# Kernel tuning notes

Hardware: AMD Instinct MI355X
Metric: run time of the kernel (lower is better)

Reference implementation:

```python
import jax, jax.numpy as jnp
import numpy as np

STRIDES = (4, 8, 16, 32)   # featmap_strides (FPN levels)
TAU = 2.0                  # level-weight temperature (translate_to_linear_weight)
G = 4                      # n_groups
SP = 32                    # spatial_points
TP = 8                     # temporal_points == T frames
D = 256                    # query_dim == feat_channels
CG = D // G                # channels per group
EFF = CG                   # eff_in_dim == eff_out_dim in AdaptiveMixing
OUT_S = SP * 4             # out_points (spatial), out_multiplier = 4
OUT_T = TP * 4
B, Q, T, IMG = 4, 100, 8, 256


def _ln2(x, eps=1e-5):
    # F.layer_norm over the last TWO dims, no affine params
    mu = jnp.mean(x, axis=(-2, -1), keepdims=True)
    var = jnp.var(x, axis=(-2, -1), keepdims=True)
    return (x - mu) * jax.lax.rsqrt(var + eps)


def _ln(x, g, b, eps=1e-5):
    mu = jnp.mean(x, axis=-1, keepdims=True)
    var = jnp.var(x, axis=-1, keepdims=True)
    return (x - mu) * jax.lax.rsqrt(var + eps) * g + b


def _bilinear(feat, px, py):
    # feat: [B,H,W,T,G,Cg]; px,py: [B,Q,G,S] pixel coords
    # grid_sample semantics: bilinear, align_corners=False, zero padding
    Bn, H, W, Tn, Gn, Cg = feat.shape
    bidx = jnp.arange(Bn)[:, None, None, None]
    gidx = jnp.arange(Gn)[None, None, :, None]
    x0 = jnp.floor(px); y0 = jnp.floor(py)
    fx = px - x0; fy = py - y0
    x0i = x0.astype(jnp.int32); y0i = y0.astype(jnp.int32)
    out = 0.0
    for dx, dy, w in ((0, 0, (1 - fx) * (1 - fy)), (1, 0, fx * (1 - fy)),
                      (0, 1, (1 - fx) * fy), (1, 1, fx * fy)):
        xi = x0i + dx; yi = y0i + dy
        valid = (xi >= 0) & (xi < W) & (yi >= 0) & (yi < H)
        xc = jnp.clip(xi, 0, W - 1); yc = jnp.clip(yi, 0, H - 1)
        v = feat[bidx, yc, xc, :, gidx, :]   # [B,Q,G,S,T,Cg]
        out = out + v * (w * valid)[..., None, None]
    return out


def _adaptive_mixing(x, query, Wp, bp, Wo, bo, n_in, n_out):
    # x: [B,Q,G,P,Cg]; per-instance dynamic channel mixing then point mixing
    Bn, Qn = x.shape[:2]
    params = (query @ Wp + bp).reshape(Bn, Qn, G, -1)
    M = params[..., :EFF * EFF].reshape(Bn, Qn, G, EFF, EFF)
    S = params[..., EFF * EFF:].reshape(Bn, Qn, G, n_out, n_in)
    out = jnp.einsum('bqgpc,bqgcd->bqgpd', x, M)
    out = jax.nn.relu(_ln2(out))
    out = jnp.einsum('bqgop,bqgpd->bqgod', S, out)
    out = jax.nn.relu(_ln2(out))
    out = out.reshape(Bn, Qn, -1) @ Wo + bo
    return query + out


def _forward(feat0, feat1, feat2, feat3, proposal_boxes, spatial_queries, temporal_queries,
             W_off, b_off, W_ps, b_ps, Wo_s, bo_s, g_s, be_s,
             W_pt, b_pt, Wo_t, bo_t, g_t, be_t):
    feats = (feat0, feat1, feat2, feat3)
    Bn, Qn, _ = spatial_queries.shape
    # offset_generator + make_sample_points (xyzr proposal boxes)
    off = (spatial_queries @ W_off + b_off).reshape(Bn, Qn, G * SP, 3)
    cc = proposal_boxes[..., None, :2]
    scale = 2.0 ** proposal_boxes[..., None, 2:3]
    r = proposal_boxes[..., None, 3:4]
    wh = scale * jnp.concatenate([2.0 ** (-0.5 * r), 2.0 ** (0.5 * r)], axis=-1)
    xy = (cc + off[..., :2] * wh).reshape(Bn, Qn, G, SP, 2)
    z = (proposal_boxes[..., None, 2] + off[..., 2]).reshape(Bn, Qn, G, SP)
    # soft level weights over log2-scale distance (translate_to_linear_weight)
    mapped = z - jnp.float32(float(np.log2(STRIDES[0])))
    lvls = jnp.arange(len(STRIDES), dtype=z.dtype)
    lw = jax.nn.softmax(-((mapped[..., None] - lvls) ** 2) / TAU, axis=-1)
    sampled = 0.0
    for i, feat in enumerate(feats):
        Bc, C, Tn, H, W = feat.shape
        fr = feat.transpose(0, 3, 4, 2, 1).reshape(Bc, H, W, Tn, G, CG)
        px = xy[..., 0] / STRIDES[i] - 0.5
        py = xy[..., 1] / STRIDES[i] - 0.5
        sampled = sampled + _bilinear(fr, px, py) * lw[..., i][..., None, None]
    sampled = sampled.transpose(0, 1, 2, 4, 3, 5)     # [B,Q,G,T,SP,Cg]
    spatial_feats = jnp.mean(sampled, axis=3)         # mean over T   -> [B,Q,G,SP,Cg]
    temporal_feats = jnp.mean(sampled, axis=4)        # mean over SP  -> [B,Q,G,T,Cg]
    sq = _adaptive_mixing(spatial_feats, spatial_queries, W_ps, b_ps, Wo_s, bo_s, SP, OUT_S)
    sq = _ln(sq, g_s, be_s)
    tq = _adaptive_mixing(temporal_feats, temporal_queries, W_pt, b_pt, Wo_t, bo_t, TP, OUT_T)
    tq = _ln(tq, g_t, be_t)
    return sq, tq


def setup_inputs() -> dict:
    key = jax.random.key(0)
    ks = jax.random.split(key, 24)
    f32 = jnp.float32
    inp = {}
    for i, s in enumerate(STRIDES):
        h = IMG // s
        inp['feat%d' % i] = jax.random.normal(ks[i], (B, D, T, h, h), dtype=f32)
    # xyzr boxes: center xy in image coords, z = log2 box scale, r = log2 aspect
    inp['proposal_boxes'] = jnp.concatenate([
        jax.random.uniform(ks[4], (B, Q, 2), dtype=f32) * IMG,
        jax.random.uniform(ks[5], (B, Q, 1), dtype=f32) * 3.0 + 3.0,
        jax.random.normal(ks[6], (B, Q, 1), dtype=f32) * 0.25,
    ], axis=-1)
    PS = EFF * EFF + SP * OUT_S
    PT = EFF * EFF + TP * OUT_T
    inp.update(
        spatial_queries=jax.random.normal(ks[7], (B, Q, D), dtype=f32),
        temporal_queries=jax.random.normal(ks[8], (B, Q, D), dtype=f32),
        W_off=jax.random.normal(ks[9], (D, SP * G * 3), dtype=f32) * 0.01,
        b_off=jax.random.normal(ks[10], (SP * G * 3,), dtype=f32) * 0.1,
        W_ps=jax.random.normal(ks[11], (D, G * PS), dtype=f32) * 0.02,
        b_ps=jax.random.normal(ks[12], (G * PS,), dtype=f32) * 0.02,
        Wo_s=jax.random.normal(ks[13], (G * EFF * OUT_S, D), dtype=f32) * 0.02,
        bo_s=jax.random.normal(ks[14], (D,), dtype=f32) * 0.02,
        g_s=jnp.ones((D,), dtype=f32),
        be_s=jnp.zeros((D,), dtype=f32),
        W_pt=jax.random.normal(ks[15], (D, G * PT), dtype=f32) * 0.02,
        b_pt=jax.random.normal(ks[16], (G * PT,), dtype=f32) * 0.02,
        Wo_t=jax.random.normal(ks[17], (G * EFF * OUT_T, D), dtype=f32) * 0.02,
        bo_t=jax.random.normal(ks[18], (D,), dtype=f32) * 0.02,
        g_t=jnp.ones((D,), dtype=f32),
        be_t=jnp.zeros((D,), dtype=f32),
    )
    return inp


def reference(feat0, feat1, feat2, feat3, proposal_boxes, spatial_queries, temporal_queries,
              W_off, b_off, W_ps, b_ps, Wo_s, bo_s, g_s, be_s,
              W_pt, b_pt, Wo_t, bo_t, g_t, be_t):
    return _forward(feat0, feat1, feat2, feat3, proposal_boxes, spatial_queries, temporal_queries,
                    W_off, b_off, W_ps, b_ps, Wo_s, bo_s, g_s, be_s,
                    W_pt, b_pt, Wo_t, bo_t, g_t, be_t)
```

## Files before the change

### kernel.cpp

```cpp
#include <hip/hip_runtime.h>
#include <hip/hip_bf16.h>


typedef __attribute__((ext_vector_type(8))) short bf16x8;
typedef __attribute__((ext_vector_type(8))) unsigned short u16x8;
typedef __attribute__((ext_vector_type(4))) float f32x4;

static __device__ __forceinline__ unsigned short f2bf(float f){
  unsigned u = __float_as_uint(f);
  u += 0x7fffu + ((u >> 16) & 1u);
  return (unsigned short)(u >> 16);
}
static __device__ __forceinline__ float bf2f(unsigned short h){
  return __uint_as_float(((unsigned)h) << 16);
}

__global__ __launch_bounds__(256) void k_wtrans_all(
    const float* __restrict__ Wps, const float* __restrict__ Wpt,
    const float* __restrict__ Wos, const float* __restrict__ Wot,
    unsigned short* __restrict__ WpsP, unsigned short* __restrict__ WptP,
    unsigned short* __restrict__ WosP, unsigned short* __restrict__ WotP,
    const float4* __restrict__ qs, const float4* __restrict__ qt,
    unsigned short* __restrict__ qsP, unsigned short* __restrict__ qtP){
  int id = blockIdx.x;
  if(id >= 5696){
    int blk = id - 5696;
    const float4* in; unsigned short* out; int i;
    if(blk < 100){ in = qs; out = qsP; i = blk*256 + threadIdx.x; }
    else         { in = qt; out = qtP; i = (blk-100)*256 + threadIdx.x; }
    float4 v = in[i];
    int row = i >> 6, k0 = (i & 63) * 4;
    int strip = row >> 4, colr = row & 15;
    int kk = k0 >> 5, kg = (k0 >> 3) & 3, e0 = k0 & 7;
    size_t dst = ((size_t)(strip*8 + kk)*64 + kg*16 + colr)*8 + e0;
    *(ushort4*)(out + dst) = make_ushort4(f2bf(v.x), f2bf(v.y), f2bf(v.z), f2bf(v.w));
    return;
  }
  const float* in; unsigned short* out; int N, KKtot, r0, c0;
  if(id < 2048){       in=Wps; out=WpsP; N=32768; KKtot=8;    c0=(id>>2)*64;        r0=(id&3)*64; }
  else if(id < 3136){ int i=id-2048; in=Wpt; out=WptP; N=17408; KKtot=8;    c0=(i>>2)*64; r0=(i&3)*64; }
  else if(id < 5184){ int i=id-3136; in=Wos; out=WosP; N=256;   KKtot=1024; c0=(i&3)*64;  r0=(i>>2)*64; }
  else {              int i=id-5184; in=Wot; out=WotP; N=256;   KKtot=256;  c0=(i&3)*64;  r0=(i>>2)*64; }
  __shared__ float tile[64][65];
  int lane = threadIdx.x & 63, wid = threadIdx.x >> 6;
  #pragma unroll
  for(int i=0;i<16;i++){
    int r = wid + 4*i;
    tile[r][lane] = in[(size_t)(r0 + r) * N + c0 + lane];
  }
  __syncthreads();
  int t = threadIdx.x;
  int ch = t >> 5, w2 = t & 31;
  int kk_l = ch >> 2, st_l = ch & 3;
  size_t chunkbase = ((size_t)((c0>>4) + st_l) * KKtot + ((r0>>5) + kk_l)) * 512;
  #pragma unroll
  for(int j=0;j<2;j++){
    int pl = w2*2 + j;
    int kg = pl >> 4, cc = pl & 15;
    u16x8 v;
    #pragma unroll
    for(int e=0;e<8;e++) v[e] = f2bf(tile[kk_l*32 + kg*8 + e][st_l*16 + cc]);
    *(u16x8*)(out + chunkbase + pl*8) = v;
  }
}

__global__ __launch_bounds__(384) void k_offsets(
    const float* __restrict__ q, const float* __restrict__ Woff,
    const float* __restrict__ boff, const float* __restrict__ boxes,
    float* __restrict__ xybuf, float* __restrict__ lwbuf){
  int bq = blockIdx.x;
  __shared__ float qsh[256];
  __shared__ float off[384];
  int tid = threadIdx.x;
  if(tid < 256) qsh[tid] = q[bq*256 + tid];
  __syncthreads();
  float acc = boff[tid];
  for(int k=0;k<256;k++) acc = fmaf(qsh[k], Woff[k*384 + tid], acc);
  off[tid] = acc;
  __syncthreads();
  if(tid < 128){
    float cx = boxes[bq*4+0], cy = boxes[bq*4+1];
    float zb = boxes[bq*4+2], r  = boxes[bq*4+3];
    float wx = exp2f(zb - 0.5f*r);
    float wy = exp2f(zb + 0.5f*r);
    float x = cx + off[tid*3+0]*wx;
    float y = cy + off[tid*3+1]*wy;
    float z = zb + off[tid*3+2];
    xybuf[(bq*128+tid)*2+0] = x;
    xybuf[(bq*128+tid)*2+1] = y;
    float m = z - 2.0f;
    float e0 = -0.5f*(m-0.f)*(m-0.f);
    float e1 = -0.5f*(m-1.f)*(m-1.f);
    float e2 = -0.5f*(m-2.f)*(m-2.f);
    float e3 = -0.5f*(m-3.f)*(m-3.f);
    float mx = fmaxf(fmaxf(e0,e1), fmaxf(e2,e3));
    float s0 = expf(e0-mx), s1 = expf(e1-mx), s2 = expf(e2-mx), s3 = expf(e3-mx);
    float inv = 1.0f/(s0+s1+s2+s3);
    lwbuf[(bq*128+tid)*4+0] = s0*inv;
    lwbuf[(bq*128+tid)*4+1] = s1*inv;
    lwbuf[(bq*128+tid)*4+2] = s2*inv;
    lwbuf[(bq*128+tid)*4+3] = s3*inv;
  }
}

__global__ __launch_bounds__(256) void k_feat_transpose_all(
    const float* __restrict__ f0, const float* __restrict__ f1,
    const float* __restrict__ f2, const float* __restrict__ f3,
    unsigned short* __restrict__ o0, unsigned short* __restrict__ o1,
    unsigned short* __restrict__ o2, unsigned short* __restrict__ o3){
  int px = blockIdx.x;
  const float* in; unsigned short* out; int P, p0;
  if(px < 64){      in=f0; out=o0; P=4096; p0=px*64; }
  else if(px < 80){ in=f1; out=o1; P=1024; p0=(px-64)*64; }
  else if(px < 84){ in=f2; out=o2; P=256;  p0=(px-80)*64; }
  else {            in=f3; out=o3; P=64;   p0=0; }
  __shared__ float tile[64][65];
  int c0 = blockIdx.y * 64;
  int b = blockIdx.z >> 3, t = blockIdx.z & 7;
  int tid = threadIdx.x;
  size_t inbase = ((size_t)b * 2048 + t) * (size_t)P;
  #pragma unroll
  for(int j=0;j<4;j++){
    int idx = j*256 + tid;
    int c = idx >> 4, q4 = idx & 15;
    float4 v = *(const float4*)(in + inbase + (size_t)(c0 + c) * 8 * P + p0 + q4*4);
    tile[c][q4*4+0] = v.x; tile[c][q4*4+1] = v.y;
    tile[c][q4*4+2] = v.z; tile[c][q4*4+3] = v.w;
  }
  __syncthreads();
  size_t outbase = (size_t)b * P * 2048 + (size_t)t * 256;
  #pragma unroll
  for(int j=0;j<4;j++){
    int idx = j*256 + tid;
    int p = idx >> 4, q4 = idx & 15;
    ushort4 o;
    o.x = f2bf(tile[q4*4+0][p]); o.y = f2bf(tile[q4*4+1][p]);
    o.z = f2bf(tile[q4*4+2][p]); o.w = f2bf(tile[q4*4+3][p]);
    *(ushort4*)(out + outbase + (size_t)(p0 + p) * 2048 + c0 + q4*4) = o;
  }
}

__global__ __launch_bounds__(256, 4) void k_sample_params(
    const unsigned short* __restrict__ f0, const unsigned short* __restrict__ f1,
    const unsigned short* __restrict__ f2, const unsigned short* __restrict__ f3,
    const float* __restrict__ xybuf, const float* __restrict__ lwbuf,
    float* __restrict__ sfeat, float* __restrict__ tfeat,
    const unsigned short* __restrict__ As, const unsigned short* __restrict__ WTs,
    const float* __restrict__ biass, unsigned short* __restrict__ outs,
    const unsigned short* __restrict__ At, const unsigned short* __restrict__ WTt,
    const float* __restrict__ biast, unsigned short* __restrict__ outt){
  if(blockIdx.x >= 1600){
    int flat = blockIdx.x - 1600;
    int nb = flat % 784, my = flat / 784;
    const unsigned short *A, *W; const float* bias; unsigned short* out; int N, nbl;
    if(nb < 512){ A=As; W=WTs; bias=biass; out=outs; N=32768; nbl=nb; }
    else        { A=At; W=WTt; bias=biast; out=outt; N=17408; nbl=nb-512; }
    int wave = threadIdx.x >> 6, lane = threadIdx.x & 63;
    int strip = nbl*4 + wave;
    int col = lane & 15, kg = lane >> 4;
    const bf16x8* wp = (const bf16x8*)W + (size_t)strip*8*64 + lane;
    bf16x8 bfrag[8];
    #pragma unroll
    for(int k=0;k<8;k++) bfrag[k] = wp[k*64];
    float bv = bias[strip*16 + col];
    int mt0 = my * 5;
    #pragma unroll
    for(int m=0; m<5; m++){
      int mt = mt0 + m;
      f32x4 acc = {bv, bv, bv, bv};
      const bf16x8* ap = (const bf16x8*)A + (size_t)mt*8*64 + lane;
      bf16x8 af[8];
      #pragma unroll
      for(int k=0;k<8;k++) af[k] = ap[k*64];
      #pragma unroll
      for(int k=0;k<8;k++)
        acc = __builtin_amdgcn_mfma_f32_16x16x32_bf16(af[k], bfrag[k], acc, 0, 0, 0);
      int rowb = mt*16 + kg*4;
      #pragma unroll
      for(int r=0;r<4;r++)
        out[(size_t)(rowb + r) * N + strip*16 + col] = f2bf(acc[r]);
    }
    return;
  }
  int bid = blockIdx.x;
  int g = bid & 3, bq = bid >> 2;
  int b = bq / 100;
  __shared__ unsigned smp[32][8][32];
  __shared__ int   soff[128][4];
  __shared__ float swt [128][4];
  int tid = threadIdx.x;
  if(tid < 128){
    int sp = tid >> 2, l = tid & 3;
    float x  = xybuf[(bq*128 + g*32 + sp)*2+0];
    float y  = xybuf[(bq*128 + g*32 + sp)*2+1];
    float lw = lwbuf[(bq*128 + g*32 + sp)*4 + l];
    float inv = (l==0) ? 0.25f : (l==1) ? 0.125f : (l==2) ? 0.0625f : 0.03125f;
    int W = 64 >> l;
    float px = x*inv - 0.5f, py = y*inv - 0.5f;
    float x0f = floorf(px), y0f = floorf(py);
    int x0 = (int)x0f, y0 = (int)y0f;
    float fx = px - x0f, fy = py - y0f;
    #pragma unroll
    for(int tap=0; tap<4; tap++){
      int dx = tap & 1, dy = tap >> 1;
      int xi = x0 + dx, yi = y0 + dy;
      bool valid = (xi >= 0) & (xi < W) & (yi >= 0) & (yi < W);
      int xc = min(max(xi, 0), W-1), yc = min(max(yi, 0), W-1);
      float w = (dx ? fx : 1.f-fx) * (dy ? fy : 1.f-fy) * lw;
      soff[tid][tap] = (yc*W + xc) * 4096;
      swt [tid][tap] = valid ? w : 0.f;
    }
  }
  __syncthreads();
  int cp = tid & 31, t = tid >> 5;
  int tcb = t*256 + g*64 + cp*2;
  const char* fb0 = (const char*)(f0 + (size_t)b*4096*2048 + tcb);
  const char* fb1 = (const char*)(f1 + (size_t)b*1024*2048 + tcb);
  const char* fb2 = (const char*)(f2 + (size_t)b* 256*2048 + tcb);
  const char* fb3 = (const char*)(f3 + (size_t)b*  64*2048 + tcb);
  float t0 = 0.f, t1 = 0.f;
  #pragma unroll 2
  for(int sp=0; sp<32; sp++){
    float a0 = 0.f, a1 = 0.f;
    #pragma unroll
    for(int l=0; l<4; l++){
      int idx = sp*4 + l;
      const char* fb = (l==0) ? fb0 : (l==1) ? fb1 : (l==2) ? fb2 : fb3;
      #pragma unroll
      for(int tap=0; tap<4; tap++){
        int off = soff[idx][tap];
        float w = swt[idx][tap];
        unsigned v = *(const unsigned*)(fb + (size_t)off);
        a0 = fmaf(w, __uint_as_float((v & 0xffffu) << 16), a0);
        a1 = fmaf(w, __uint_as_float(v & 0xffff0000u),      a1);
      }
    }
    smp[sp][t][cp] = (unsigned)f2bf(a0) | ((unsigned)f2bf(a1) << 16);
    t0 += a0; t1 += a1;
  }
  __syncthreads();
  {
    size_t o = ((size_t)(bq*4 + g)*8 + t)*64 + cp*2;
    tfeat[o+0] = t0 * (1.f/32.f);
    tfeat[o+1] = t1 * (1.f/32.f);
  }
  #pragma unroll
  for(int i=0;i<4;i++){
    int j = tid + 256*i;
    int sp = j >> 5, p = j & 31;
    float s0 = 0.f, s1 = 0.f;
    #pragma unroll
    for(int tt=0; tt<8; tt++){
      unsigned v = smp[sp][tt][p];
      s0 += __uint_as_float((v & 0xffffu) << 16);
      s1 += __uint_as_float(v & 0xffff0000u);
    }
    size_t o = ((size_t)(bq*4 + g)*32 + sp)*64 + p*2;
    sfeat[o+0] = s0 * 0.125f;
    sfeat[o+1] = s1 * 0.125f;
  }
}

static __device__ __forceinline__ void block_reduce2(
    float& s1, float& s2, float* rA, float* rB, int tid){
  #pragma unroll
  for(int o=32;o;o>>=1){ s1 += __shfl_xor(s1,o); s2 += __shfl_xor(s2,o); }
  int wave = tid >> 6, lane = tid & 63;
  if(lane == 0){ rA[wave] = s1; rB[wave] = s2; }
  __syncthreads();
  s1 = rA[0]+rA[1]+rA[2]+rA[3];
  s2 = rB[0]+rB[1]+rB[2]+rB[3];
}

template<int P, int O>
__global__ __launch_bounds__(256) void k_mix(
    const float* __restrict__ feats, const unsigned short* __restrict__ params,
    unsigned short* __restrict__ hidden, int KK){
  int bid = blockIdx.x; int g = bid & 3, bq = bid >> 2;
  const int PG = 4096 + O*P;
  const unsigned short* pp = params + (size_t)bq * 4 * PG + (size_t)g * PG;
  const float* xin = feats + (size_t)(bq*4 + g) * P * 64;
  __shared__ float xs[P][64];
  __shared__ float o1[P][64];
  __shared__ float Ss[O*P];
  __shared__ float rA[4], rB[4];
  int tid = threadIdx.x; int d = tid & 63; int pb = tid >> 6;
  for(int i=tid; i<P*64; i+=256) xs[i>>6][i&63] = xin[i];
  for(int i=tid; i<O*P; i+=256) Ss[i] = bf2f(pp[4096 + i]);
  __syncthreads();
  constexpr int NP = P/4;
  float a[NP];
  #pragma unroll
  for(int i=0;i<NP;i++) a[i] = 0.f;
  for(int c=0;c<64;c++){
    float mv = bf2f(pp[c*64 + d]);
    #pragma unroll
    for(int i=0;i<NP;i++) a[i] = fmaf(xs[pb + 4*i][c], mv, a[i]);
  }
  float s1 = 0.f, s2 = 0.f;
  #pragma unroll
  for(int i=0;i<NP;i++){ s1 += a[i]; s2 += a[i]*a[i]; }
  block_reduce2(s1, s2, rA, rB, tid);
  {
    const float n = (float)(P*64);
    float mu = s1/n, var = s2/n - mu*mu;
    float rstd = rsqrtf(var + 1e-5f);
    #pragma unroll
    for(int i=0;i<NP;i++){
      float v = (a[i] - mu) * rstd;
      o1[pb + 4*i][d] = fmaxf(v, 0.f);
    }
  }
  __syncthreads();
  constexpr int NO = O/4;
  float bacc[NO];
  #pragma unroll
  for(int i=0;i<NO;i++){
    float acc = 0.f;
    int o = pb + 4*i;
    #pragma unroll
    for(int p=0;p<P;p++) acc = fmaf(Ss[o*P + p], o1[p][d], acc);
    bacc[i] = acc;
  }
  s1 = 0.f; s2 = 0.f;
  #pragma unroll
  for(int i=0;i<NO;i++){ s1 += bacc[i]; s2 += bacc[i]*bacc[i]; }
  block_reduce2(s1, s2, rA, rB, tid);
  {
    const float n = (float)(O*64);
    float mu = s1/n, var = s2/n - mu*mu;
    float rstd = rsqrtf(var + 1e-5f);
    int strip = bq >> 4, colr = bq & 15;
    int kg = (d >> 3) & 3, e = d & 7, dh = d >> 5;
    #pragma unroll
    for(int i=0;i<NO;i++){
      int o = pb + 4*i;
      float v = (bacc[i] - mu) * rstd;
      int kk = (g*O + o)*2 + dh;
      size_t addr = ((size_t)(strip*KK + kk)*64 + kg*16 + colr)*8 + e;
      hidden[addr] = f2bf(fmaxf(v, 0.f));
    }
  }
}

__global__ __launch_bounds__(256, 4) void k_gemm_final(
    const unsigned short* __restrict__ Hs, const unsigned short* __restrict__ WTs,
    float* __restrict__ parts, const unsigned short* __restrict__ Ht,
    const unsigned short* __restrict__ WTt, float* __restrict__ partt){
  const unsigned short *H, *W; float* partial; int KK, ks, ksteps;
  if(blockIdx.x < 64){ H=Hs; W=WTs; partial=parts; KK=1024; ks=blockIdx.x;    ksteps=16; }
  else               { H=Ht; W=WTt; partial=partt; KK=256;  ks=blockIdx.x-64; ksteps=4;  }
  int wave = threadIdx.x >> 6, lane = threadIdx.x & 63;
  int col = lane & 15, kg = lane >> 4;
  int mt = blockIdx.y;
  int kk0 = ks * ksteps;
  int n0 = wave * 64;
  f32x4 acc[4] = {};
  const bf16x8* ap  = (const bf16x8*)H + ((size_t)mt*KK + kk0)*64 + lane;
  const bf16x8* bp0 = (const bf16x8*)W + ((size_t)(4*wave+0)*KK + kk0)*64 + lane;
  const bf16x8* bp1 = (const bf16x8*)W + ((size_t)(4*wave+1)*KK + kk0)*64 + lane;
  const bf16x8* bp2 = (const bf16x8*)W + ((size_t)(4*wave+2)*KK + kk0)*64 + lane;
  const bf16x8* bp3 = (const bf16x8*)W + ((size_t)(4*wave+3)*KK + kk0)*64 + lane;
  #pragma unroll 4
  for(int kk=0; kk<ksteps; kk++){
    bf16x8 af = ap[kk*64];
    bf16x8 b0 = bp0[kk*64], b1 = bp1[kk*64], b2 = bp2[kk*64], b3 = bp3[kk*64];
    acc[0] = __builtin_amdgcn_mfma_f32_16x16x32_bf16(af, b0, acc[0], 0,0,0);
    acc[1] = __builtin_amdgcn_mfma_f32_16x16x32_bf16(af, b1, acc[1], 0,0,0);
    acc[2] = __builtin_amdgcn_mfma_f32_16x16x32_bf16(af, b2, acc[2], 0,0,0);
    acc[3] = __builtin_amdgcn_mfma_f32_16x16x32_bf16(af, b3, acc[3], 0,0,0);
  }
  int rowb = mt*16 + kg*4;
  #pragma unroll
  for(int nt=0; nt<4; nt++)
    #pragma unroll
    for(int r=0; r<4; r++)
      partial[((size_t)ks*400 + rowb + r)*256 + n0 + nt*16 + col] = acc[nt][r];
}

template<int NS>
__global__ __launch_bounds__(256) void k_finalize(
    const float* __restrict__ part_s, const float* __restrict__ part_t,
    const float* __restrict__ qs, const float* __restrict__ qt,
    const float* __restrict__ bos, const float* __restrict__ bot,
    const float* __restrict__ gs, const float* __restrict__ gt,
    const float* __restrict__ bes, const float* __restrict__ bet,
    float* __restrict__ out_s, float* __restrict__ out_t){
  __shared__ float rA[4], rB[4];
  int bq = blockIdx.x, j = threadIdx.x;
  const float *partial, *q, *bo, *gam, *bet_;
  float* out;
  if(blockIdx.y == 0){ partial=part_s; q=qs; bo=bos; gam=gs; bet_=bes; out=out_s; }
  else               { partial=part_t; q=qt; bo=bot; gam=gt; bet_=bet; out=out_t; }
  float v = q[bq*256 + j] + bo[j];
  #pragma unroll 8
  for(int s=0;s<NS;s++) v += partial[((size_t)s*400 + bq)*256 + j];
  float s1 = v, s2 = v*v;
  block_reduce2(s1, s2, rA, rB, j);
  float mu = s1 * (1.f/256.f);
  float var = s2 * (1.f/256.f) - mu*mu;
  float rstd = rsqrtf(var + 1e-5f);
  out[bq*256 + j] = (v - mu) * rstd * gam[j] + bet_[j];
}

extern "C" void kernel_launch(void* const* d_in, const int* in_sizes, int n_in,
                              void* d_out, int out_size, void* d_ws, size_t ws_size,
                              hipStream_t stream){
  const float* feat0 = (const float*)d_in[0];
  const float* feat1 = (const float*)d_in[1];
  const float* feat2 = (const float*)d_in[2];
  const float* feat3 = (const float*)d_in[3];
  const float* boxes = (const float*)d_in[4];
  const float* qs    = (const float*)d_in[5];
  const float* qt    = (const float*)d_in[6];
  const float* Woff  = (const float*)d_in[7];
  const float* boff  = (const float*)d_in[8];
  const float* Wps   = (const float*)d_in[9];
  const float* bps   = (const float*)d_in[10];
  const float* Wos   = (const float*)d_in[11];
  const float* bos   = (const float*)d_in[12];
  const float* gs    = (const float*)d_in[13];
  const float* bes   = (const float*)d_in[14];
  const float* Wpt   = (const float*)d_in[15];
  const float* bpt   = (const float*)d_in[16];
  const float* Wot   = (const float*)d_in[17];
  const float* bot   = (const float*)d_in[18];
  const float* gt    = (const float*)d_in[19];
  const float* bet   = (const float*)d_in[20];

  char* ws = (char*)d_ws;
  unsigned short* featT0 = (unsigned short*)(ws + 0);
  unsigned short* featT1 = (unsigned short*)(ws + 67108864);
  unsigned short* featT2 = (unsigned short*)(ws + 83886080);
  unsigned short* featT3 = (unsigned short*)(ws + 88080384);
  float* part_s          = (float*)(ws + 0);
  float* part_t          = (float*)(ws + 52428800);
  unsigned short* qsP    = (unsigned short*)(ws + 89128960);
  unsigned short* qtP    = (unsigned short*)(ws + 89333760);
  unsigned short* WpsP   = (unsigned short*)(ws + 89538560);
  unsigned short* WptP   = (unsigned short*)(ws + 106315776);
  unsigned short* WosP   = (unsigned short*)(ws + 115228672);
  unsigned short* WotP   = (unsigned short*)(ws + 132005888);
  float* xybuf           = (float*)(ws + 136232960);
  float* lwbuf           = (float*)(ws + 136642560);
  float* sfeat           = (float*)(ws + 137461760);
  float* tfeat           = (float*)(ws + 150568960);
  unsigned short* hid_s  = (unsigned short*)(ws + 153845760);
  unsigned short* hid_t  = (unsigned short*)(ws + 180060160);
  unsigned short* params_s = (unsigned short*)(ws + 186613760);
  unsigned short* params_t = (unsigned short*)(ws + 212828160);
  float* out_s = (float*)d_out;
  float* out_t = out_s + 102400;

  k_wtrans_all<<<5896, 256, 0, stream>>>(Wps, Wpt, Wos, Wot, WpsP, WptP, WosP, WotP,
                                         (const float4*)qs, (const float4*)qt, qsP, qtP);
  k_feat_transpose_all<<<dim3(85, 4, 32), 256, 0, stream>>>(
      feat0, feat1, feat2, feat3, featT0, featT1, featT2, featT3);
  k_offsets<<<400, 384, 0, stream>>>(qs, Woff, boff, boxes, xybuf, lwbuf);
  k_sample_params<<<5520, 256, 0, stream>>>(featT0, featT1, featT2, featT3,
                                            xybuf, lwbuf, sfeat, tfeat,
                                            qsP, WpsP, bps, params_s,
                                            qtP, WptP, bpt, params_t);
  k_mix<32,128><<<1600, 256, 0, stream>>>(sfeat, params_s, hid_s, 1024);
  k_mix< 8, 32><<<1600, 256, 0, stream>>>(tfeat, params_t, hid_t, 256);
  k_gemm_final<<<dim3(128, 25), 256, 0, stream>>>(hid_s, WosP, part_s,
                                                  hid_t, WotP, part_t);
  k_finalize<64><<<dim3(400, 2), 256, 0, stream>>>(
      part_s, part_t, qs, qt, bos, bot, gs, gt, bes, bet, out_s, out_t);
}
```

Before: 279.3 us.

## Merge prep kernels and mix kernels into single launches; halve GEMM split-K

The offsets, feature transpose and weight/query packing kernels are folded into one k_prep_all launch with a shared smem buffer, and the two k_mix instantiations become one k_mix_all launch dispatched by block index. The final GEMM's split-K factor is halved, so each block runs twice as many k-steps, and finalize reduces fewer partials. The aim is to cut launch gaps and tail effects and to shrink partial-sum traffic. The cost is fewer GEMM blocks (less parallelism) and a larger shared footprint for the temporal mix blocks, which may lower occupancy.

New measurement: 325.2 us. 16.4% more time.

```diff
diff --git a/kernel.cpp b/kernel.cpp
--- a/kernel.cpp
+++ b/kernel.cpp
@@ -15,128 +15,143 @@
   return __uint_as_float(((unsigned)h) << 16);
 }
 
-__global__ __launch_bounds__(256) void k_wtrans_all(
+__global__ __launch_bounds__(256) void k_prep_all(
+    const float* __restrict__ qsf, const float* __restrict__ Woff,
+    const float* __restrict__ boff, const float* __restrict__ boxes,
+    float* __restrict__ xybuf, float* __restrict__ lwbuf,
+    const float* __restrict__ f0, const float* __restrict__ f1,
+    const float* __restrict__ f2, const float* __restrict__ f3,
+    unsigned short* __restrict__ o0, unsigned short* __restrict__ o1,
+    unsigned short* __restrict__ o2, unsigned short* __restrict__ o3,
     const float* __restrict__ Wps, const float* __restrict__ Wpt,
     const float* __restrict__ Wos, const float* __restrict__ Wot,
     unsigned short* __restrict__ WpsP, unsigned short* __restrict__ WptP,
     unsigned short* __restrict__ WosP, unsigned short* __restrict__ WotP,
-    const float4* __restrict__ qs, const float4* __restrict__ qt,
+    const float4* __restrict__ qs4, const float4* __restrict__ qt4,
     unsigned short* __restrict__ qsP, unsigned short* __restrict__ qtP){
+  __shared__ float shp[64*65];
   int id = blockIdx.x;
-  if(id >= 5696){
-    int blk = id - 5696;
+  int tid = threadIdx.x;
+
+  if(id < 400){
+    int bq = id;
+    float* qsh = shp;
+    float* off = shp + 256;
+    qsh[tid] = qsf[bq*256 + tid];
+    __syncthreads();
+    float acc0 = boff[tid];
+    bool has2 = tid < 128;
+    float acc1 = has2 ? boff[256 + tid] : 0.f;
+    for(int k=0;k<256;k++){
+      float qv = qsh[k];
+      acc0 = fmaf(qv, Woff[k*384 + tid], acc0);
+      if(has2) acc1 = fmaf(qv, Woff[k*384 + 256 + tid], acc1);
+    }
+    off[tid] = acc0;
+    if(has2) off[256 + tid] = acc1;
+    __syncthreads();
+    if(tid < 128){
+      float cx = boxes[bq*4+0], cy = boxes[bq*4+1];
+      float zb = boxes[bq*4+2], r  = boxes[bq*4+3];
+      float wx = exp2f(zb - 0.5f*r);
+      float wy = exp2f(zb + 0.5f*r);
+      float x = cx + off[tid*3+0]*wx;
+      float y = cy + off[tid*3+1]*wy;
+      float z = zb + off[tid*3+2];
+      xybuf[(bq*128+tid)*2+0] = x;
+      xybuf[(bq*128+tid)*2+1] = y;
+      float m = z - 2.0f;
+      float e0 = -0.5f*(m-0.f)*(m-0.f);
+      float e1 = -0.5f*(m-1.f)*(m-1.f);
+      float e2 = -0.5f*(m-2.f)*(m-2.f);
+      float e3 = -0.5f*(m-3.f)*(m-3.f);
+      float mx = fmaxf(fmaxf(e0,e1), fmaxf(e2,e3));
+      float s0 = expf(e0-mx), s1 = expf(e1-mx), s2 = expf(e2-mx), s3 = expf(e3-mx);
+      float inv = 1.0f/(s0+s1+s2+s3);
+      lwbuf[(bq*128+tid)*4+0] = s0*inv;
+      lwbuf[(bq*128+tid)*4+1] = s1*inv;
+      lwbuf[(bq*128+tid)*4+2] = s2*inv;
+      lwbuf[(bq*128+tid)*4+3] = s3*inv;
+    }
+    return;
+  }
+
+  if(id < 11280){
+    int i = id - 400;
+    int px = i % 85, rest = i / 85;
+    int c0 = (rest & 3) * 64;
+    int z = rest >> 2;
+    int b = z >> 3, t = z & 7;
+    const float* in; unsigned short* out; int P, p0;
+    if(px < 64){      in=f0; out=o0; P=4096; p0=px*64; }
+    else if(px < 80){ in=f1; out=o1; P=1024; p0=(px-64)*64; }
+    else if(px < 84){ in=f2; out=o2; P=256;  p0=(px-80)*64; }
+    else {            in=f3; out=o3; P=64;   p0=0; }
+    float (*tile)[65] = (float(*)[65])shp;
+    size_t inbase = ((size_t)b * 2048 + t) * (size_t)P;
+    #pragma unroll
+    for(int j=0;j<4;j++){
+      int idx = j*256 + tid;
+      int c = idx >> 4, q4 = idx & 15;
+      float4 v = *(const float4*)(in + inbase + (size_t)(c0 + c) * 8 * P + p0 + q4*4);
+      tile[c][q4*4+0] = v.x; tile[c][q4*4+1] = v.y;
+      tile[c][q4*4+2] = v.z; tile[c][q4*4+3] = v.w;
+    }
+    __syncthreads();
+    size_t outbase = (size_t)b * P * 2048 + (size_t)t * 256;
+    #pragma unroll
+    for(int j=0;j<4;j++){
+      int idx = j*256 + tid;
+      int p = idx >> 4, q4 = idx & 15;
+      ushort4 o;
+      o.x = f2bf(tile[q4*4+0][p]); o.y = f2bf(tile[q4*4+1][p]);
+      o.z = f2bf(tile[q4*4+2][p]); o.w = f2bf(tile[q4*4+3][p]);
+      *(ushort4*)(out + outbase + (size_t)(p0 + p) * 2048 + c0 + q4*4) = o;
+    }
+    return;
+  }
+
+  if(id < 16976){
+    int wi = id - 11280;
+    const float* in; unsigned short* out; int N, KKtot, r0, c0;
+    if(wi < 2048){       in=Wps; out=WpsP; N=32768; KKtot=8;    c0=(wi>>2)*64;        r0=(wi&3)*64; }
+    else if(wi < 3136){ int i2=wi-2048; in=Wpt; out=WptP; N=17408; KKtot=8;    c0=(i2>>2)*64; r0=(i2&3)*64; }
+    else if(wi < 5184){ int i2=wi-3136; in=Wos; out=WosP; N=256;   KKtot=1024; c0=(i2&3)*64;  r0=(i2>>2)*64; }
+    else {              int i2=wi-5184; in=Wot; out=WotP; N=256;   KKtot=256;  c0=(i2&3)*64;  r0=(i2>>2)*64; }
+    float (*tile)[65] = (float(*)[65])shp;
+    int lane = tid & 63, wid = tid >> 6;
+    #pragma unroll
+    for(int i2=0;i2<16;i2++){
+      int r = wid + 4*i2;
+      tile[r][lane] = in[(size_t)(r0 + r) * N + c0 + lane];
+    }
+    __syncthreads();
+    int ch = tid >> 5, w2 = tid & 31;
+    int kk_l = ch >> 2, st_l = ch & 3;
+    size_t chunkbase = ((size_t)((c0>>4) + st_l) * KKtot + ((r0>>5) + kk_l)) * 512;
+    #pragma unroll
+    for(int j=0;j<2;j++){
+      int pl = w2*2 + j;
+      int kg = pl >> 4, cc = pl & 15;
+      u16x8 v;
+      #pragma unroll
+      for(int e=0;e<8;e++) v[e] = f2bf(tile[kk_l*32 + kg*8 + e][st_l*16 + cc]);
+      *(u16x8*)(out + chunkbase + pl*8) = v;
+    }
+    return;
+  }
+
+  {
+    int blk = id - 16976;
     const float4* in; unsigned short* out; int i;
-    if(blk < 100){ in = qs; out = qsP; i = blk*256 + threadIdx.x; }
-    else         { in = qt; out = qtP; i = (blk-100)*256 + threadIdx.x; }
+    if(blk < 100){ in = qs4; out = qsP; i = blk*256 + tid; }
+    else         { in = qt4; out = qtP; i = (blk-100)*256 + tid; }
     float4 v = in[i];
     int row = i >> 6, k0 = (i & 63) * 4;
     int strip = row >> 4, colr = row & 15;
     int kk = k0 >> 5, kg = (k0 >> 3) & 3, e0 = k0 & 7;
     size_t dst = ((size_t)(strip*8 + kk)*64 + kg*16 + colr)*8 + e0;
     *(ushort4*)(out + dst) = make_ushort4(f2bf(v.x), f2bf(v.y), f2bf(v.z), f2bf(v.w));
-    return;
-  }
-  const float* in; unsigned short* out; int N, KKtot, r0, c0;
-  if(id < 2048){       in=Wps; out=WpsP; N=32768; KKtot=8;    c0=(id>>2)*64;        r0=(id&3)*64; }
-  else if(id < 3136){ int i=id-2048; in=Wpt; out=WptP; N=17408; KKtot=8;    c0=(i>>2)*64; r0=(i&3)*64; }
-  else if(id < 5184){ int i=id-3136; in=Wos; out=WosP; N=256;   KKtot=1024; c0=(i&3)*64;  r0=(i>>2)*64; }
-  else {              int i=id-5184; in=Wot; out=WotP; N=256;   KKtot=256;  c0=(i&3)*64;  r0=(i>>2)*64; }
-  __shared__ float tile[64][65];
-  int lane = threadIdx.x & 63, wid = threadIdx.x >> 6;
-  #pragma unroll
-  for(int i=0;i<16;i++){
-    int r = wid + 4*i;
-    tile[r][lane] = in[(size_t)(r0 + r) * N + c0 + lane];
-  }
-  __syncthreads();
-  int t = threadIdx.x;
-  int ch = t >> 5, w2 = t & 31;
-  int kk_l = ch >> 2, st_l = ch & 3;
-  size_t chunkbase = ((size_t)((c0>>4) + st_l) * KKtot + ((r0>>5) + kk_l)) * 512;
-  #pragma unroll
-  for(int j=0;j<2;j++){
-    int pl = w2*2 + j;
-    int kg = pl >> 4, cc = pl & 15;
-    u16x8 v;
-    #pragma unroll
-    for(int e=0;e<8;e++) v[e] = f2bf(tile[kk_l*32 + kg*8 + e][st_l*16 + cc]);
-    *(u16x8*)(out + chunkbase + pl*8) = v;
-  }
-}
-
-__global__ __launch_bounds__(384) void k_offsets(
-    const float* __restrict__ q, const float* __restrict__ Woff,
-    const float* __restrict__ boff, const float* __restrict__ boxes,
-    float* __restrict__ xybuf, float* __restrict__ lwbuf){
-  int bq = blockIdx.x;
-  __shared__ float qsh[256];
-  __shared__ float off[384];
-  int tid = threadIdx.x;
-  if(tid < 256) qsh[tid] = q[bq*256 + tid];
-  __syncthreads();
-  float acc = boff[tid];
-  for(int k=0;k<256;k++) acc = fmaf(qsh[k], Woff[k*384 + tid], acc);
-  off[tid] = acc;
-  __syncthreads();
-  if(tid < 128){
-    float cx = boxes[bq*4+0], cy = boxes[bq*4+1];
-    float zb = boxes[bq*4+2], r  = boxes[bq*4+3];
-    float wx = exp2f(zb - 0.5f*r);
-    float wy = exp2f(zb + 0.5f*r);
-    float x = cx + off[tid*3+0]*wx;
-    float y = cy + off[tid*3+1]*wy;
-    float z = zb + off[tid*3+2];
-    xybuf[(bq*128+tid)*2+0] = x;
-    xybuf[(bq*128+tid)*2+1] = y;
-    float m = z - 2.0f;
-    float e0 = -0.5f*(m-0.f)*(m-0.f);
-    float e1 = -0.5f*(m-1.f)*(m-1.f);
-    float e2 = -0.5f*(m-2.f)*(m-2.f);
-    float e3 = -0.5f*(m-3.f)*(m-3.f);
-    float mx = fmaxf(fmaxf(e0,e1), fmaxf(e2,e3));
-    float s0 = expf(e0-mx), s1 = expf(e1-mx), s2 = expf(e2-mx), s3 = expf(e3-mx);
-    float inv = 1.0f/(s0+s1+s2+s3);
-    lwbuf[(bq*128+tid)*4+0] = s0*inv;
-    lwbuf[(bq*128+tid)*4+1] = s1*inv;
-    lwbuf[(bq*128+tid)*4+2] = s2*inv;
-    lwbuf[(bq*128+tid)*4+3] = s3*inv;
-  }
-}
-
-__global__ __launch_bounds__(256) void k_feat_transpose_all(
-    const float* __restrict__ f0, const float* __restrict__ f1,
-    const float* __restrict__ f2, const float* __restrict__ f3,
-    unsigned short* __restrict__ o0, unsigned short* __restrict__ o1,
-    unsigned short* __restrict__ o2, unsigned short* __restrict__ o3){
-  int px = blockIdx.x;
-  const float* in; unsigned short* out; int P, p0;
-  if(px < 64){      in=f0; out=o0; P=4096; p0=px*64; }
-  else if(px < 80){ in=f1; out=o1; P=1024; p0=(px-64)*64; }
-  else if(px < 84){ in=f2; out=o2; P=256;  p0=(px-80)*64; }
-  else {            in=f3; out=o3; P=64;   p0=0; }
-  __shared__ float tile[64][65];
-  int c0 = blockIdx.y * 64;
-  int b = blockIdx.z >> 3, t = blockIdx.z & 7;
-  int tid = threadIdx.x;
-  size_t inbase = ((size_t)b * 2048 + t) * (size_t)P;
-  #pragma unroll
-  for(int j=0;j<4;j++){
-    int idx = j*256 + tid;
-    int c = idx >> 4, q4 = idx & 15;
-    float4 v = *(const float4*)(in + inbase + (size_t)(c0 + c) * 8 * P + p0 + q4*4);
-    tile[c][q4*4+0] = v.x; tile[c][q4*4+1] = v.y;
-    tile[c][q4*4+2] = v.z; tile[c][q4*4+3] = v.w;
-  }
-  __syncthreads();
-  size_t outbase = (size_t)b * P * 2048 + (size_t)t * 256;
-  #pragma unroll
-  for(int j=0;j<4;j++){
-    int idx = j*256 + tid;
-    int p = idx >> 4, q4 = idx & 15;
-    ushort4 o;
-    o.x = f2bf(tile[q4*4+0][p]); o.y = f2bf(tile[q4*4+1][p]);
-    o.z = f2bf(tile[q4*4+2][p]); o.w = f2bf(tile[q4*4+3][p]);
-    *(ushort4*)(out + outbase + (size_t)(p0 + p) * 2048 + c0 + q4*4) = o;
   }
 }
 
@@ -273,17 +288,19 @@
 }
 
 template<int P, int O>
-__global__ __launch_bounds__(256) void k_mix(
-    const float* __restrict__ feats, const unsigned short* __restrict__ params,
-    unsigned short* __restrict__ hidden, int KK){
-  int bid = blockIdx.x; int g = bid & 3, bq = bid >> 2;
+static __device__ void mix_body(
+    float* shbuf, const float* __restrict__ feats,
+    const unsigned short* __restrict__ params,
+    unsigned short* __restrict__ hidden, int KK, int bid){
+  int g = bid & 3, bq = bid >> 2;
   const int PG = 4096 + O*P;
   const unsigned short* pp = params + (size_t)bq * 4 * PG + (size_t)g * PG;
   const float* xin = feats + (size_t)(bq*4 + g) * P * 64;
-  __shared__ float xs[P][64];
-  __shared__ float o1[P][64];
-  __shared__ float Ss[O*P];
-  __shared__ float rA[4], rB[4];
+  float (*xs)[64] = (float(*)[64])shbuf;
+  float (*o1)[64] = (float(*)[64])(shbuf + P*64);
+  float* Ss = shbuf + 2*P*64;
+  float* rA = shbuf + 2*P*64 + O*P;
+  float* rB = rA + 4;
   int tid = threadIdx.x; int d = tid & 63; int pb = tid >> 6;
   for(int i=tid; i<P*64; i+=256) xs[i>>6][i&63] = xin[i];
   for(int i=tid; i<O*P; i+=256) Ss[i] = bf2f(pp[4096 + i]);
@@ -343,13 +360,25 @@
   }
 }
 
+__global__ __launch_bounds__(256) void k_mix_all(
+    const float* __restrict__ sfeat, const unsigned short* __restrict__ params_s,
+    unsigned short* __restrict__ hid_s,
+    const float* __restrict__ tfeat, const unsigned short* __restrict__ params_t,
+    unsigned short* __restrict__ hid_t){
+  __shared__ float shbuf[2*32*64 + 128*32 + 8];
+  if(blockIdx.x < 1600)
+    mix_body<32,128>(shbuf, sfeat, params_s, hid_s, 1024, blockIdx.x);
+  else
+    mix_body<8,32>(shbuf, tfeat, params_t, hid_t, 256, blockIdx.x - 1600);
+}
+
 __global__ __launch_bounds__(256, 4) void k_gemm_final(
     const unsigned short* __restrict__ Hs, const unsigned short* __restrict__ WTs,
     float* __restrict__ parts, const unsigned short* __restrict__ Ht,
     const unsigned short* __restrict__ WTt, float* __restrict__ partt){
   const unsigned short *H, *W; float* partial; int KK, ks, ksteps;
-  if(blockIdx.x < 64){ H=Hs; W=WTs; partial=parts; KK=1024; ks=blockIdx.x;    ksteps=16; }
-  else               { H=Ht; W=WTt; partial=partt; KK=256;  ks=blockIdx.x-64; ksteps=4;  }
+  if(blockIdx.x < 32){ H=Hs; W=WTs; partial=parts; KK=1024; ks=blockIdx.x;    ksteps=32; }
+  else               { H=Ht; W=WTt; partial=partt; KK=256;  ks=blockIdx.x-32; ksteps=8;  }
   int wave = threadIdx.x >> 6, lane = threadIdx.x & 63;
   int col = lane & 15, kg = lane >> 4;
   int mt = blockIdx.y;
@@ -452,19 +481,19 @@
   float* out_s = (float*)d_out;
   float* out_t = out_s + 102400;
 
-  k_wtrans_all<<<5896, 256, 0, stream>>>(Wps, Wpt, Wos, Wot, WpsP, WptP, WosP, WotP,
-                                         (const float4*)qs, (const float4*)qt, qsP, qtP);
-  k_feat_transpose_all<<<dim3(85, 4, 32), 256, 0, stream>>>(
-      feat0, feat1, feat2, feat3, featT0, featT1, featT2, featT3);
-  k_offsets<<<400, 384, 0, stream>>>(qs, Woff, boff, boxes, xybuf, lwbuf);
+  k_prep_all<<<17176, 256, 0, stream>>>(
+      qs, Woff, boff, boxes, xybuf, lwbuf,
+      feat0, feat1, feat2, feat3, featT0, featT1, featT2, featT3,
+      Wps, Wpt, Wos, Wot, WpsP, WptP, WosP, WotP,
+      (const float4*)qs, (const float4*)qt, qsP, qtP);
   k_sample_params<<<5520, 256, 0, stream>>>(featT0, featT1, featT2, featT3,
                                             xybuf, lwbuf, sfeat, tfeat,
                                             qsP, WpsP, bps, params_s,
                                             qtP, WptP, bpt, params_t);
-  k_mix<32,128><<<1600, 256, 0, stream>>>(sfeat, params_s, hid_s, 1024);
-  k_mix< 8, 32><<<1600, 256, 0, stream>>>(tfeat, params_t, hid_t, 256);
-  k_gemm_final<<<dim3(128, 25), 256, 0, stream>>>(hid_s, WosP, part_s,
-                                                  hid_t, WotP, part_t);
-  k_finalize<64><<<dim3(400, 2), 256, 0, stream>>>(
+  k_mix_all<<<3200, 256, 0, stream>>>(sfeat, params_s, hid_s,
+                                      tfeat, params_t, hid_t);
+  k_gemm_final<<<dim3(64, 25), 256, 0, stream>>>(hid_s, WosP, part_s,
+                                                 hid_t, WotP, part_t);
+  k_finalize<32><<<dim3(400, 2), 256, 0, stream>>>(
       part_s, part_t, qs, qt, bos, bot, gs, gt, bes, bet, out_s, out_t);
 }
```

## Merge mix kernels, halve GEMM split-K, simplify feature transpose indexing

Applied to the files above, without the earlier changes.

The two adaptive-mixing launches become one kernel that picks the spatial or temporal body by block index and shares a single shared-memory buffer, which removes one launch and lets the two workloads overlap. The final GEMM's split-K factor is halved, so each block does twice as many k-steps and half as many partial sums go to the finalize kernel. The feature transpose now uses scalar per-lane loads and 2-byte stores in place of float4 loads and ushort4 stores. That may cut LDS bank conflicts but also narrows global memory transactions. The merged mix kernel sizes shared memory for the larger spatial case, which may lower occupancy for the temporal blocks.

Measured after the change: 281.7 us. Within noise of the previous version (+0.9%).

```diff
diff --git a/kernel.cpp b/kernel.cpp
--- a/kernel.cpp
+++ b/kernel.cpp
@@ -117,26 +117,19 @@
   __shared__ float tile[64][65];
   int c0 = blockIdx.y * 64;
   int b = blockIdx.z >> 3, t = blockIdx.z & 7;
-  int tid = threadIdx.x;
+  int lane = threadIdx.x & 63, wid = threadIdx.x >> 6;
   size_t inbase = ((size_t)b * 2048 + t) * (size_t)P;
   #pragma unroll
-  for(int j=0;j<4;j++){
-    int idx = j*256 + tid;
-    int c = idx >> 4, q4 = idx & 15;
-    float4 v = *(const float4*)(in + inbase + (size_t)(c0 + c) * 8 * P + p0 + q4*4);
-    tile[c][q4*4+0] = v.x; tile[c][q4*4+1] = v.y;
-    tile[c][q4*4+2] = v.z; tile[c][q4*4+3] = v.w;
+  for(int i=0;i<16;i++){
+    int c = wid + 4*i;
+    tile[c][lane] = in[inbase + (size_t)(c0 + c) * 8 * P + p0 + lane];
   }
   __syncthreads();
   size_t outbase = (size_t)b * P * 2048 + (size_t)t * 256;
   #pragma unroll
-  for(int j=0;j<4;j++){
-    int idx = j*256 + tid;
-    int p = idx >> 4, q4 = idx & 15;
-    ushort4 o;
-    o.x = f2bf(tile[q4*4+0][p]); o.y = f2bf(tile[q4*4+1][p]);
-    o.z = f2bf(tile[q4*4+2][p]); o.w = f2bf(tile[q4*4+3][p]);
-    *(ushort4*)(out + outbase + (size_t)(p0 + p) * 2048 + c0 + q4*4) = o;
+  for(int i=0;i<16;i++){
+    int p = wid + 4*i;
+    out[outbase + (size_t)(p0 + p) * 2048 + c0 + lane] = f2bf(tile[lane][p]);
   }
 }
 
@@ -273,17 +266,19 @@
 }
 
 template<int P, int O>
-__global__ __launch_bounds__(256) void k_mix(
-    const float* __restrict__ feats, const unsigned short* __restrict__ params,
-    unsigned short* __restrict__ hidden, int KK){
-  int bid = blockIdx.x; int g = bid & 3, bq = bid >> 2;
+static __device__ void mix_body(
+    float* shbuf, const float* __restrict__ feats,
+    const unsigned short* __restrict__ params,
+    unsigned short* __restrict__ hidden, int KK, int bid){
+  int g = bid & 3, bq = bid >> 2;
   const int PG = 4096 + O*P;
   const unsigned short* pp = params + (size_t)bq * 4 * PG + (size_t)g * PG;
   const float* xin = feats + (size_t)(bq*4 + g) * P * 64;
-  __shared__ float xs[P][64];
-  __shared__ float o1[P][64];
-  __shared__ float Ss[O*P];
-  __shared__ float rA[4], rB[4];
+  float (*xs)[64] = (float(*)[64])shbuf;
+  float (*o1)[64] = (float(*)[64])(shbuf + P*64);
+  float* Ss = shbuf + 2*P*64;
+  float* rA = shbuf + 2*P*64 + O*P;
+  float* rB = rA + 4;
   int tid = threadIdx.x; int d = tid & 63; int pb = tid >> 6;
   for(int i=tid; i<P*64; i+=256) xs[i>>6][i&63] = xin[i];
   for(int i=tid; i<O*P; i+=256) Ss[i] = bf2f(pp[4096 + i]);
@@ -343,13 +338,25 @@
   }
 }
 
+__global__ __launch_bounds__(256) void k_mix_all(
+    const float* __restrict__ sfeat, const unsigned short* __restrict__ params_s,
+    unsigned short* __restrict__ hid_s,
+    const float* __restrict__ tfeat, const unsigned short* __restrict__ params_t,
+    unsigned short* __restrict__ hid_t){
+  __shared__ float shbuf[2*32*64 + 128*32 + 8];
+  if(blockIdx.x < 1600)
+    mix_body<32,128>(shbuf, sfeat, params_s, hid_s, 1024, blockIdx.x);
+  else
+    mix_body<8,32>(shbuf, tfeat, params_t, hid_t, 256, blockIdx.x - 1600);
+}
+
 __global__ __launch_bounds__(256, 4) void k_gemm_final(
     const unsigned short* __restrict__ Hs, const unsigned short* __restrict__ WTs,
     float* __restrict__ parts, const unsigned short* __restrict__ Ht,
     const unsigned short* __restrict__ WTt, float* __restrict__ partt){
   const unsigned short *H, *W; float* partial; int KK, ks, ksteps;
-  if(blockIdx.x < 64){ H=Hs; W=WTs; partial=parts; KK=1024; ks=blockIdx.x;    ksteps=16; }
-  else               { H=Ht; W=WTt; partial=partt; KK=256;  ks=blockIdx.x-64; ksteps=4;  }
+  if(blockIdx.x < 32){ H=Hs; W=WTs; partial=parts; KK=1024; ks=blockIdx.x;    ksteps=32; }
+  else               { H=Ht; W=WTt; partial=partt; KK=256;  ks=blockIdx.x-32; ksteps=8;  }
   int wave = threadIdx.x >> 6, lane = threadIdx.x & 63;
   int col = lane & 15, kg = lane >> 4;
   int mt = blockIdx.y;
@@ -461,10 +468,10 @@
                                             xybuf, lwbuf, sfeat, tfeat,
                                             qsP, WpsP, bps, params_s,
                                             qtP, WptP, bpt, params_t);
-  k_mix<32,128><<<1600, 256, 0, stream>>>(sfeat, params_s, hid_s, 1024);
-  k_mix< 8, 32><<<1600, 256, 0, stream>>>(tfeat, params_t, hid_t, 256);
-  k_gemm_final<<<dim3(128, 25), 256, 0, stream>>>(hid_s, WosP, part_s,
-                                                  hid_t, WotP, part_t);
-  k_finalize<64><<<dim3(400, 2), 256, 0, stream>>>(
+  k_mix_all<<<3200, 256, 0, stream>>>(sfeat, params_s, hid_s,
+                                      tfeat, params_t, hid_t);
+  k_gemm_final<<<dim3(64, 25), 256, 0, stream>>>(hid_s, WosP, part_s,
+                                                 hid_t, WotP, part_t);
+  k_finalize<32><<<dim3(400, 2), 256, 0, stream>>>(
       part_s, part_t, qs, qt, bos, bot, gs, gt, bes, bet, out_s, out_t);
 }
```
